# Kernel tuning notes

Measured on AMD Instinct MI355X. Metric: run time of the kernel, lower is better.

The kernel has to match this reference:

```python
import jax, jax.numpy as jnp
import numpy as np

B, T, N, E, H, MAXD = 32, 128, 42, 256, 8, 7
DH = E // H


def _hand_edges():
    left = [(0, 1), (1, 2), (2, 3), (3, 4), (0, 5), (5, 6), (6, 7), (7, 8), (0, 9), (9, 10), (10, 11), (11, 12), (0, 13), (13, 14), (14, 15), (15, 16), (0, 17), (17, 18), (18, 19), (19, 20)]
    right = [(21, 22), (22, 23), (23, 24), (24, 25), (21, 26), (26, 27), (27, 28), (28, 29), (21, 30), (30, 31), (31, 32), (32, 33), (21, 34), (34, 35), (35, 36), (36, 37), (21, 38), (38, 39), (39, 40), (40, 41)]
    tips = [(4, 8), (8, 12), (12, 16), (16, 20), (25, 29), (29, 33), (33, 37), (37, 41)]
    cross = [(0, 21)]
    return left + right + cross + tips


def _graph_constants():
    adj = np.zeros((N, N), dtype=np.float32)
    dist = np.zeros((N, N), dtype=np.float64)
    for a, b in _hand_edges():
        adj[a, b] = 1.0
        adj[b, a] = 1.0
        dist[a, b] = 1.0
        dist[b, a] = 1.0
    # exact replica of the module's single-pass Floyd-Warshall-style loop
    for k in range(N):
        for i in range(N):
            for j in range(N):
                if i != j and dist[i, k] > 0 and dist[k, j] > 0:
                    nd = dist[i, k] + dist[k, j]
                    if dist[i, j] == 0 or nd < dist[i, j]:
                        dist[i, j] = nd
    dist = np.clip(dist, 0, MAXD).astype(np.int32)
    return adj, dist


def setup_inputs() -> dict:
    key = jax.random.key(0)
    ks = jax.random.split(key, 12)
    adj_np, dist_np = _graph_constants()
    s_in = 1.0 / np.sqrt(E)
    return {
        'node_features': jax.random.normal(ks[0], (B, T, N, E), dtype=jnp.float32),
        'adjacency_matrix': jnp.asarray(adj_np),
        'distances': jnp.asarray(dist_np),
        'Wq': jax.random.normal(ks[1], (E, E), dtype=jnp.float32) * s_in,
        'bq': jnp.zeros((E,), dtype=jnp.float32),
        'Wk': jax.random.normal(ks[2], (E, E), dtype=jnp.float32) * s_in,
        'bk': jnp.zeros((E,), dtype=jnp.float32),
        'Wv': jax.random.normal(ks[3], (E, E), dtype=jnp.float32) * s_in,
        'bv': jnp.zeros((E,), dtype=jnp.float32),
        'Wo': jax.random.normal(ks[4], (E, E), dtype=jnp.float32) * s_in,
        'bo': jnp.zeros((E,), dtype=jnp.float32),
        'rel_emb': jax.random.normal(ks[5], (2 * MAXD + 1, H), dtype=jnp.float32) * 0.05,
    }


def reference(node_features, adjacency_matrix, distances, Wq, bq, Wk, bk, Wv, bv, Wo, bo, rel_emb):
    b, t, n, e = node_features.shape
    q = (node_features @ Wq + bq).reshape(b, t, n, H, DH)
    k = (node_features @ Wk + bk).reshape(b, t, n, H, DH)
    v = (node_features @ Wv + bv).reshape(b, t, n, H, DH)
    # scores: [b, t, h, i, j]
    scores = jnp.einsum('btihd,btjhd->bthij', q, k) / jnp.sqrt(jnp.float32(DH))
    # relative position bias: [n, n, h] -> [h, n, n]
    bias = rel_emb[distances]  # (N, N, H)
    scores = scores + jnp.transpose(bias, (2, 0, 1))[None, None]
    mask = (adjacency_matrix > 0).astype(jnp.float32)[None, None, None]
    scores = scores * mask + (1.0 - mask) * (-1e9)
    attn = jax.nn.softmax(scores, axis=-1)
    out = jnp.einsum('bthij,btjhd->btihd', attn, v).reshape(b, t, n, e)
    out = out @ Wo + bo
    return out, attn
```

## Files before the change

### kernel.cpp

```cpp
#include <hip/hip_runtime.h>
#include <stdint.h>


#define TPB 512
constexpr int BT = 4096;
constexpr int N = 42, NP = 48, E = 256, H = 8, DH = 32;
constexpr int NE = N * E;
constexpr int NN = N * N;
constexpr float SCALE = 0.17677669529663687f;

typedef short sh8 __attribute__((ext_vector_type(8)));
typedef float f4 __attribute__((ext_vector_type(4)));

__device__ __forceinline__ float b2f(uint16_t u) {
  union { uint32_t i; float f; } v; v.i = ((uint32_t)u) << 16; return v.f;
}
__device__ __forceinline__ uint16_t f2b(float f) {
  union { float f; uint32_t i; } v; v.f = f;
  const uint32_t x = v.i;
  return (uint16_t)((x + 0x7fffu + ((x >> 16) & 1u)) >> 16);
}

#define SWZ(base, row, cb) \
  ((char*)(base) + ((((row) << 9) + (cb)) ^ (((row) & 7) << 4)))

__global__ __launch_bounds__(256) void wt_kernel(
    const float* __restrict__ Wq, const float* __restrict__ Wk,
    const float* __restrict__ Wv, const float* __restrict__ Wo,
    uint16_t* __restrict__ WT) {
  __shared__ float tl[32][33];
  const int z = blockIdx.z;
  const float* W = (z == 0) ? Wq : (z == 1) ? Wk : (z == 2) ? Wv : Wo;
  uint16_t* dst = WT + z * 65536;
  const int k0 = blockIdx.y * 32, n0 = blockIdx.x * 32;
  const int r = threadIdx.x >> 5, cc = threadIdx.x & 31;
#pragma unroll
  for (int p = 0; p < 4; ++p)
    tl[r + 8 * p][cc] = W[(k0 + r + 8 * p) * E + n0 + cc];
  __syncthreads();
#pragma unroll
  for (int p = 0; p < 4; ++p)
    dst[(n0 + r + 8 * p) * E + k0 + cc] = f2b(tl[cc][r + 8 * p]);
}

__global__ __launch_bounds__(TPB, 4) void gt_kernel(
    const float* __restrict__ X, const float* __restrict__ adj,
    const int* __restrict__ dist,
    const float* __restrict__ bq, const float* __restrict__ bk,
    const float* __restrict__ bv, const float* __restrict__ bo,
    const float* __restrict__ rel, const uint16_t* __restrict__ WT,
    float* __restrict__ out, float* __restrict__ attn) {
  alignas(16) __shared__ char smem[76512];
  uint16_t* const Xb = (uint16_t*)smem;
  uint16_t* const VT = (uint16_t*)smem;
  uint16_t* const Qb = (uint16_t*)(smem + 24576);
  uint16_t* const Kb = (uint16_t*)(smem + 49152);
  uint16_t* const Ps = (uint16_t*)(smem + 24576);
  uint8_t*  const dm8 = (uint8_t*)(smem + 73728);
  float*    const relL = (float*)(smem + 76032);

  const int gid = blockIdx.x;
  const int tid = threadIdx.x;
  const int w = tid >> 6, lane = tid & 63, c = lane & 15, lg = lane >> 4;

  const uint16_t* WTq = WT;
  const uint16_t* WTk = WT + 65536;
  const uint16_t* WTv = WT + 131072;
  const uint16_t* WTo = WT + 196608;

  {
    const float2* Xs = (const float2*)(X + (size_t)gid * NE);
    for (int i = tid; i < NE / 2; i += TPB) {
      const float2 v = Xs[i];
      const int row = i >> 7, cb = (i & 127) << 2;
      const uint32_t pk = (uint32_t)f2b(v.x) | ((uint32_t)f2b(v.y) << 16);
      *(uint32_t*)SWZ(Xb, row, cb) = pk;
    }
    for (int i = tid; i < (NP - N) * 128; i += TPB) {
      const int row = N + (i >> 7), cb = (i & 127) << 2;
      *(uint32_t*)SWZ(Xb, row, cb) = 0u;
    }
    for (int t = tid; t < NP * NP; t += TPB) {
      const int i = t / NP, j = t - i * NP;
      uint8_t v = 0;
      if (i < N && j < N) {
        const float a = adj[i * N + j];
        const int d = dist[i * N + j];
        v = (uint8_t)d | (a > 0.f ? 0x80 : 0);
      }
      dm8[t] = v;
    }
    for (int t = tid; t < 120; t += TPB) relL[t] = rel[t];
  }
  __syncthreads();

  const int nt0 = 2 * w;
  f4 aQ[3][2], aK[3][2], aV[3][2];
#pragma unroll
  for (int mt = 0; mt < 3; ++mt)
#pragma unroll
    for (int nt = 0; nt < 2; ++nt) {
      aQ[mt][nt] = (f4){0.f, 0.f, 0.f, 0.f};
      aK[mt][nt] = (f4){0.f, 0.f, 0.f, 0.f};
      aV[mt][nt] = (f4){0.f, 0.f, 0.f, 0.f};
    }
  for (int kc = 0; kc < E; kc += 32) {
    sh8 xa[3];
#pragma unroll
    for (int mt = 0; mt < 3; ++mt)
      xa[mt] = *(const sh8*)SWZ(Xb, 16 * mt + c, (kc + 8 * lg) * 2);
#pragma unroll
    for (int nt = 0; nt < 2; ++nt) {
      const int n = (nt0 + nt) * 16 + c;
      const int ko = n * E + kc + 8 * lg;
      const sh8 bq8 = *(const sh8*)(WTq + ko);
      const sh8 bk8 = *(const sh8*)(WTk + ko);
      const sh8 bv8 = *(const sh8*)(WTv + ko);
#pragma unroll
      for (int mt = 0; mt < 3; ++mt) {
        aQ[mt][nt] = __builtin_amdgcn_mfma_f32_16x16x32_bf16(xa[mt], bq8, aQ[mt][nt], 0, 0, 0);
        aK[mt][nt] = __builtin_amdgcn_mfma_f32_16x16x32_bf16(xa[mt], bk8, aK[mt][nt], 0, 0, 0);
        aV[mt][nt] = __builtin_amdgcn_mfma_f32_16x16x32_bf16(xa[mt], bv8, aV[mt][nt], 0, 0, 0);
      }
    }
  }
  __syncthreads();

#pragma unroll
  for (int nt = 0; nt < 2; ++nt) {
    const int n = (nt0 + nt) * 16 + c;
    const float bqv = bq[n], bkv = bk[n], bvv = bv[n];
#pragma unroll
    for (int mt = 0; mt < 3; ++mt) {
      uint16_t vr[4];
#pragma unroll
      for (int r = 0; r < 4; ++r) {
        const int i = 16 * mt + 4 * lg + r;
        *(uint16_t*)SWZ(Qb, i, n * 2) = f2b(aQ[mt][nt][r] + bqv);
        *(uint16_t*)SWZ(Kb, i, n * 2) = f2b(aK[mt][nt][r] + bkv);
        vr[r] = f2b(aV[mt][nt][r] + bvv);
      }
      ushort4 vv; vv.x = vr[0]; vv.y = vr[1]; vv.z = vr[2]; vv.w = vr[3];
      *(ushort4*)(VT + n * 48 + 16 * mt + 4 * lg) = vv;
    }
  }
  __syncthreads();

  {
    const int h = w;
    sh8 qa[3], kb8[3];
#pragma unroll
    for (int t = 0; t < 3; ++t) {
      qa[t] = *(const sh8*)SWZ(Qb, 16 * t + c, (h * 32 + 8 * lg) * 2);
      kb8[t] = *(const sh8*)SWZ(Kb, 16 * t + c, (h * 32 + 8 * lg) * 2);
    }
    __syncthreads();

    f4 st[3][3];
#pragma unroll
    for (int mt = 0; mt < 3; ++mt)
#pragma unroll
      for (int nt = 0; nt < 3; ++nt) {
        st[mt][nt] = (f4){0.f, 0.f, 0.f, 0.f};
        st[mt][nt] = __builtin_amdgcn_mfma_f32_16x16x32_bf16(qa[mt], kb8[nt], st[mt][nt], 0, 0, 0);
      }

    uint16_t* Psw = Ps + w * 2688;
#pragma unroll
    for (int mt = 0; mt < 3; ++mt)
#pragma unroll
      for (int r = 0; r < 4; ++r) {
        const int i = 16 * mt + 4 * lg + r;
        float sv[3];
#pragma unroll
        for (int nt = 0; nt < 3; ++nt) {
          const int j = 16 * nt + c;
          const uint8_t dm = dm8[i * NP + j];
          sv[nt] = (dm & 0x80) ? st[mt][nt][r] * SCALE + relL[(dm & 0x7f) * 8 + h]
                               : -1e9f;
        }
        float m = fmaxf(fmaxf(sv[0], sv[1]), sv[2]);
        m = fmaxf(m, __shfl_xor(m, 1));
        m = fmaxf(m, __shfl_xor(m, 2));
        m = fmaxf(m, __shfl_xor(m, 4));
        m = fmaxf(m, __shfl_xor(m, 8));
        float p0 = __expf(sv[0] - m), p1 = __expf(sv[1] - m), p2 = __expf(sv[2] - m);
        float sum = p0 + p1 + p2;
        sum += __shfl_xor(sum, 1);
        sum += __shfl_xor(sum, 2);
        sum += __shfl_xor(sum, 4);
        sum += __shfl_xor(sum, 8);
        const float inv = __builtin_amdgcn_rcpf(sum);
        Psw[i * 56 + 16 * 0 + c] = f2b(p0 * inv);
        Psw[i * 56 + 16 * 1 + c] = f2b(p1 * inv);
        Psw[i * 56 + 16 * 2 + c] = f2b(p2 * inv);
      }

    {
      const size_t abase = ((size_t)gid * H + h) * (size_t)NN;
      for (int p = lane; p < NN; p += 64) {
        const int i = p / N, j = p - i * N;
        attn[abase + p] = b2f(Psw[i * 56 + j]);
      }
    }

    const sh8 z8 = {0, 0, 0, 0, 0, 0, 0, 0};
    sh8 pa0[3], pa1[3], vb0[2], vb1[2];
#pragma unroll
    for (int mt = 0; mt < 3; ++mt) {
      pa0[mt] = *(const sh8*)(Psw + (16 * mt + c) * 56 + 8 * lg);
      pa1[mt] = (lg < 2) ? *(const sh8*)(Psw + (16 * mt + c) * 56 + 32 + 8 * lg) : z8;
    }
#pragma unroll
    for (int nt = 0; nt < 2; ++nt) {
      const int d = h * 32 + 16 * nt + c;
      vb0[nt] = *(const sh8*)(VT + d * 48 + 8 * lg);
      vb1[nt] = (lg < 2) ? *(const sh8*)(VT + d * 48 + 32 + 8 * lg) : z8;
    }
    f4 ov[3][2];
#pragma unroll
    for (int mt = 0; mt < 3; ++mt)
#pragma unroll
      for (int nt = 0; nt < 2; ++nt) {
        ov[mt][nt] = (f4){0.f, 0.f, 0.f, 0.f};
        ov[mt][nt] = __builtin_amdgcn_mfma_f32_16x16x32_bf16(pa0[mt], vb0[nt], ov[mt][nt], 0, 0, 0);
        ov[mt][nt] = __builtin_amdgcn_mfma_f32_16x16x32_bf16(pa1[mt], vb1[nt], ov[mt][nt], 0, 0, 0);
      }
    __syncthreads();
#pragma unroll
    for (int mt = 0; mt < 3; ++mt)
#pragma unroll
      for (int nt = 0; nt < 2; ++nt)
#pragma unroll
        for (int r = 0; r < 4; ++r) {
          const int i = 16 * mt + 4 * lg + r;
          const int dn = h * 32 + 16 * nt + c;
          *(uint16_t*)SWZ(Xb, i, dn * 2) = f2b(ov[mt][nt][r]);
        }
  }
  __syncthreads();

  {
    f4 ao[3][2];
#pragma unroll
    for (int mt = 0; mt < 3; ++mt)
#pragma unroll
      for (int nt = 0; nt < 2; ++nt) ao[mt][nt] = (f4){0.f, 0.f, 0.f, 0.f};
    for (int kc = 0; kc < E; kc += 32) {
      sh8 xa[3];
#pragma unroll
      for (int mt = 0; mt < 3; ++mt)
        xa[mt] = *(const sh8*)SWZ(Xb, 16 * mt + c, (kc + 8 * lg) * 2);
#pragma unroll
      for (int nt = 0; nt < 2; ++nt) {
        const int n = (nt0 + nt) * 16 + c;
        const sh8 b8 = *(const sh8*)(WTo + n * E + kc + 8 * lg);
#pragma unroll
        for (int mt = 0; mt < 3; ++mt)
          ao[mt][nt] = __builtin_amdgcn_mfma_f32_16x16x32_bf16(xa[mt], b8, ao[mt][nt], 0, 0, 0);
      }
    }
#pragma unroll
    for (int nt = 0; nt < 2; ++nt) {
      const int n = (nt0 + nt) * 16 + c;
      const float bov = bo[n];
#pragma unroll
      for (int mt = 0; mt < 3; ++mt)
#pragma unroll
        for (int r = 0; r < 4; ++r) {
          const int i = 16 * mt + 4 * lg + r;
          if (i < N) out[(size_t)gid * NE + i * E + n] = ao[mt][nt][r] + bov;
        }
    }
  }
}

extern "C" void kernel_launch(void* const* d_in, const int* in_sizes, int n_in,
                              void* d_out, int out_size, void* d_ws, size_t ws_size,
                              hipStream_t stream) {
  const float* X    = (const float*)d_in[0];
  const float* adj  = (const float*)d_in[1];
  const int*   dist = (const int*)d_in[2];
  const float* Wq   = (const float*)d_in[3];
  const float* bq   = (const float*)d_in[4];
  const float* Wk   = (const float*)d_in[5];
  const float* bk   = (const float*)d_in[6];
  const float* Wv   = (const float*)d_in[7];
  const float* bv   = (const float*)d_in[8];
  const float* Wo   = (const float*)d_in[9];
  const float* bo   = (const float*)d_in[10];
  const float* rel  = (const float*)d_in[11];
  float* out  = (float*)d_out;
  float* attn = out + (size_t)BT * NE;
  uint16_t* WT = (uint16_t*)d_ws;

  wt_kernel<<<dim3(8, 8, 4), dim3(256), 0, stream>>>(Wq, Wk, Wv, Wo, WT);
  gt_kernel<<<dim3(BT), dim3(TPB), 0, stream>>>(
      X, adj, dist, bq, bk, bv, bo, rel, WT, out, attn);
}
```

Baseline: 439.6 us.

## Split QKV projection into sequential passes with per-wave Q/K transpose scratch

The fused QKV projection that held three accumulator sets is replaced by three sequential GEMM passes. Each Q and K result is transposed through a small per-wave LDS scratch straight into MFMA fragments, which removes the shared Q/K buffers and one block barrier and cuts LDS use. The score MFMA is transposed (K times Q) so each lane holds a whole row slice and softmax needs only two cross-lane shuffles. Bf16 conversion now uses the hardware v_cvt_pk_bf16_f32 instruction, and X is loaded as float4. The attn store is moved after the PV MFMAs, and it still reads Psw with the old 56-element row stride, which matches the new 112-byte row pitch.

Result: slower. 535.7 us (+21.9%).

```diff
diff --git a/kernel.cpp b/kernel.cpp
--- a/kernel.cpp
+++ b/kernel.cpp
@@ -4,7 +4,7 @@
 
 #define TPB 512
 constexpr int BT = 4096;
-constexpr int N = 42, NP = 48, E = 256, H = 8, DH = 32;
+constexpr int N = 42, NP = 48, E = 256, H = 8;
 constexpr int NE = N * E;
 constexpr int NN = N * N;
 constexpr float SCALE = 0.17677669529663687f;
@@ -12,13 +12,14 @@
 typedef short sh8 __attribute__((ext_vector_type(8)));
 typedef float f4 __attribute__((ext_vector_type(4)));
 
+__device__ __forceinline__ uint32_t cvtpk(float lo, float hi) {
+  uint32_t d;
+  asm("v_cvt_pk_bf16_f32 %0, %1, %2" : "=v"(d) : "v"(lo), "v"(hi));
+  return d;
+}
+__device__ __forceinline__ uint16_t f2b1(float f) { return (uint16_t)cvtpk(f, f); }
 __device__ __forceinline__ float b2f(uint16_t u) {
   union { uint32_t i; float f; } v; v.i = ((uint32_t)u) << 16; return v.f;
-}
-__device__ __forceinline__ uint16_t f2b(float f) {
-  union { float f; uint32_t i; } v; v.f = f;
-  const uint32_t x = v.i;
-  return (uint16_t)((x + 0x7fffu + ((x >> 16) & 1u)) >> 16);
 }
 
 #define SWZ(base, row, cb) \
@@ -40,7 +41,45 @@
   __syncthreads();
 #pragma unroll
   for (int p = 0; p < 4; ++p)
-    dst[(n0 + r + 8 * p) * E + k0 + cc] = f2b(tl[cc][r + 8 * p]);
+    dst[(n0 + r + 8 * p) * E + k0 + cc] = f2b1(tl[cc][r + 8 * p]);
+}
+
+__device__ __forceinline__ void gemm_pass(const uint16_t* __restrict__ Wt,
+                                          const char* Xb, int c, int lg, int nt0,
+                                          f4 acc[3][2]) {
+#pragma unroll
+  for (int mt = 0; mt < 3; ++mt)
+#pragma unroll
+    for (int nt = 0; nt < 2; ++nt) acc[mt][nt] = (f4){0.f, 0.f, 0.f, 0.f};
+  for (int kc = 0; kc < E; kc += 32) {
+    sh8 xa[3];
+#pragma unroll
+    for (int mt = 0; mt < 3; ++mt)
+      xa[mt] = *(const sh8*)SWZ(Xb, 16 * mt + c, (kc + 8 * lg) * 2);
+#pragma unroll
+    for (int nt = 0; nt < 2; ++nt) {
+      const sh8 b8 = *(const sh8*)(Wt + ((nt0 + nt) * 16 + c) * E + kc + 8 * lg);
+#pragma unroll
+      for (int mt = 0; mt < 3; ++mt)
+        acc[mt][nt] = __builtin_amdgcn_mfma_f32_16x16x32_bf16(xa[mt], b8, acc[mt][nt], 0, 0, 0);
+    }
+  }
+}
+
+__device__ __forceinline__ void tr_qk(const f4 acc[3][2], const float* __restrict__ bias,
+                                      int n0, int c, int lg, uint16_t* scr, sh8 fr[3]) {
+#pragma unroll
+  for (int nt = 0; nt < 2; ++nt) {
+    const float bv = bias[n0 + 16 * nt + c];
+#pragma unroll
+    for (int mt = 0; mt < 3; ++mt)
+#pragma unroll
+      for (int r = 0; r < 4; ++r)
+        scr[(16 * mt + 4 * lg + r) * 40 + 16 * nt + c] = f2b1(acc[mt][nt][r] + bv);
+  }
+#pragma unroll
+  for (int mt = 0; mt < 3; ++mt)
+    fr[mt] = *(const sh8*)(scr + (16 * mt + c) * 40 + 8 * lg);
 }
 
 __global__ __launch_bounds__(TPB, 4) void gt_kernel(
@@ -50,43 +89,35 @@
     const float* __restrict__ bv, const float* __restrict__ bo,
     const float* __restrict__ rel, const uint16_t* __restrict__ WT,
     float* __restrict__ out, float* __restrict__ attn) {
-  alignas(16) __shared__ char smem[76512];
-  uint16_t* const Xb = (uint16_t*)smem;
+  alignas(16) __shared__ char smem[70368];
+  char* const Xb = smem;
   uint16_t* const VT = (uint16_t*)smem;
-  uint16_t* const Qb = (uint16_t*)(smem + 24576);
-  uint16_t* const Kb = (uint16_t*)(smem + 49152);
-  uint16_t* const Ps = (uint16_t*)(smem + 24576);
-  uint8_t*  const dm8 = (uint8_t*)(smem + 73728);
-  float*    const relL = (float*)(smem + 76032);
+  uint8_t*  const dm8 = (uint8_t*)(smem + 67584);
+  float*    const relL = (float*)(smem + 69888);
 
   const int gid = blockIdx.x;
   const int tid = threadIdx.x;
   const int w = tid >> 6, lane = tid & 63, c = lane & 15, lg = lane >> 4;
-
-  const uint16_t* WTq = WT;
-  const uint16_t* WTk = WT + 65536;
-  const uint16_t* WTv = WT + 131072;
-  const uint16_t* WTo = WT + 196608;
-
-  {
-    const float2* Xs = (const float2*)(X + (size_t)gid * NE);
-    for (int i = tid; i < NE / 2; i += TPB) {
-      const float2 v = Xs[i];
-      const int row = i >> 7, cb = (i & 127) << 2;
-      const uint32_t pk = (uint32_t)f2b(v.x) | ((uint32_t)f2b(v.y) << 16);
-      *(uint32_t*)SWZ(Xb, row, cb) = pk;
-    }
-    for (int i = tid; i < (NP - N) * 128; i += TPB) {
-      const int row = N + (i >> 7), cb = (i & 127) << 2;
-      *(uint32_t*)SWZ(Xb, row, cb) = 0u;
+  const int nt0 = 2 * w, n0 = 32 * w;
+  uint16_t* const scr = (uint16_t*)(smem + 24576 + w * 5376);
+
+  {
+    const float4* Xs = (const float4*)(X + (size_t)gid * NE);
+    for (int i = tid; i < NE / 4; i += TPB) {
+      const float4 v = Xs[i];
+      uint2 pk; pk.x = cvtpk(v.x, v.y); pk.y = cvtpk(v.z, v.w);
+      *(uint2*)SWZ(Xb, i >> 6, (i & 63) << 3) = pk;
+    }
+    for (int i = tid; i < (NP - N) * 32; i += TPB) {
+      uint2 z; z.x = 0u; z.y = 0u;
+      *(uint2*)SWZ(Xb, N + (i >> 5), (i & 31) << 3) = z;
     }
     for (int t = tid; t < NP * NP; t += TPB) {
       const int i = t / NP, j = t - i * NP;
       uint8_t v = 0;
       if (i < N && j < N) {
         const float a = adj[i * N + j];
-        const int d = dist[i * N + j];
-        v = (uint8_t)d | (a > 0.f ? 0x80 : 0);
+        v = (uint8_t)dist[i * N + j] | (a > 0.f ? 0x80 : 0);
       }
       dm8[t] = v;
     }
@@ -94,113 +125,74 @@
   }
   __syncthreads();
 
-  const int nt0 = 2 * w;
-  f4 aQ[3][2], aK[3][2], aV[3][2];
-#pragma unroll
-  for (int mt = 0; mt < 3; ++mt)
-#pragma unroll
-    for (int nt = 0; nt < 2; ++nt) {
-      aQ[mt][nt] = (f4){0.f, 0.f, 0.f, 0.f};
-      aK[mt][nt] = (f4){0.f, 0.f, 0.f, 0.f};
-      aV[mt][nt] = (f4){0.f, 0.f, 0.f, 0.f};
-    }
-  for (int kc = 0; kc < E; kc += 32) {
-    sh8 xa[3];
-#pragma unroll
-    for (int mt = 0; mt < 3; ++mt)
-      xa[mt] = *(const sh8*)SWZ(Xb, 16 * mt + c, (kc + 8 * lg) * 2);
-#pragma unroll
-    for (int nt = 0; nt < 2; ++nt) {
-      const int n = (nt0 + nt) * 16 + c;
-      const int ko = n * E + kc + 8 * lg;
-      const sh8 bq8 = *(const sh8*)(WTq + ko);
-      const sh8 bk8 = *(const sh8*)(WTk + ko);
-      const sh8 bv8 = *(const sh8*)(WTv + ko);
-#pragma unroll
-      for (int mt = 0; mt < 3; ++mt) {
-        aQ[mt][nt] = __builtin_amdgcn_mfma_f32_16x16x32_bf16(xa[mt], bq8, aQ[mt][nt], 0, 0, 0);
-        aK[mt][nt] = __builtin_amdgcn_mfma_f32_16x16x32_bf16(xa[mt], bk8, aK[mt][nt], 0, 0, 0);
-        aV[mt][nt] = __builtin_amdgcn_mfma_f32_16x16x32_bf16(xa[mt], bv8, aV[mt][nt], 0, 0, 0);
-      }
-    }
-  }
+  sh8 qa[3], kb[3];
+  {
+    f4 acc[3][2];
+    gemm_pass(WT, Xb, c, lg, nt0, acc);
+    tr_qk(acc, bq, n0, c, lg, scr, qa);
+    gemm_pass(WT + 65536, Xb, c, lg, nt0, acc);
+    tr_qk(acc, bk, n0, c, lg, scr, kb);
+  }
+  f4 av[3][2];
+  gemm_pass(WT + 131072, Xb, c, lg, nt0, av);
   __syncthreads();
 
 #pragma unroll
   for (int nt = 0; nt < 2; ++nt) {
-    const int n = (nt0 + nt) * 16 + c;
-    const float bqv = bq[n], bkv = bk[n], bvv = bv[n];
+    const int n = n0 + 16 * nt + c;
+    const float bvv = bv[n];
 #pragma unroll
     for (int mt = 0; mt < 3; ++mt) {
-      uint16_t vr[4];
-#pragma unroll
-      for (int r = 0; r < 4; ++r) {
-        const int i = 16 * mt + 4 * lg + r;
-        *(uint16_t*)SWZ(Qb, i, n * 2) = f2b(aQ[mt][nt][r] + bqv);
-        *(uint16_t*)SWZ(Kb, i, n * 2) = f2b(aK[mt][nt][r] + bkv);
-        vr[r] = f2b(aV[mt][nt][r] + bvv);
-      }
-      ushort4 vv; vv.x = vr[0]; vv.y = vr[1]; vv.z = vr[2]; vv.w = vr[3];
-      *(ushort4*)(VT + n * 48 + 16 * mt + 4 * lg) = vv;
-    }
-  }
-  __syncthreads();
+      uint2 pk;
+      pk.x = cvtpk(av[mt][nt][0] + bvv, av[mt][nt][1] + bvv);
+      pk.y = cvtpk(av[mt][nt][2] + bvv, av[mt][nt][3] + bvv);
+      *(uint2*)((char*)VT + n * 96 + 32 * mt + 8 * lg) = pk;
+    }
+  }
 
   {
     const int h = w;
-    sh8 qa[3], kb8[3];
-#pragma unroll
-    for (int t = 0; t < 3; ++t) {
-      qa[t] = *(const sh8*)SWZ(Qb, 16 * t + c, (h * 32 + 8 * lg) * 2);
-      kb8[t] = *(const sh8*)SWZ(Kb, 16 * t + c, (h * 32 + 8 * lg) * 2);
-    }
-    __syncthreads();
-
     f4 st[3][3];
 #pragma unroll
     for (int mt = 0; mt < 3; ++mt)
 #pragma unroll
       for (int nt = 0; nt < 3; ++nt) {
         st[mt][nt] = (f4){0.f, 0.f, 0.f, 0.f};
-        st[mt][nt] = __builtin_amdgcn_mfma_f32_16x16x32_bf16(qa[mt], kb8[nt], st[mt][nt], 0, 0, 0);
-      }
-
-    uint16_t* Psw = Ps + w * 2688;
-#pragma unroll
-    for (int mt = 0; mt < 3; ++mt)
-#pragma unroll
-      for (int r = 0; r < 4; ++r) {
-        const int i = 16 * mt + 4 * lg + r;
-        float sv[3];
-#pragma unroll
-        for (int nt = 0; nt < 3; ++nt) {
-          const int j = 16 * nt + c;
+        st[mt][nt] = __builtin_amdgcn_mfma_f32_16x16x32_bf16(kb[mt], qa[nt], st[mt][nt], 0, 0, 0);
+      }
+
+    uint16_t* const Psw = scr;
+#pragma unroll
+    for (int nt = 0; nt < 3; ++nt) {
+      const int i = 16 * nt + c;
+      float sv[12];
+#pragma unroll
+      for (int mt = 0; mt < 3; ++mt)
+#pragma unroll
+        for (int r = 0; r < 4; ++r) {
+          const int j = 16 * mt + 4 * lg + r;
           const uint8_t dm = dm8[i * NP + j];
-          sv[nt] = (dm & 0x80) ? st[mt][nt][r] * SCALE + relL[(dm & 0x7f) * 8 + h]
-                               : -1e9f;
+          const float s = st[mt][nt][r] * SCALE + relL[(dm & 0x7f) * 8 + h];
+          sv[mt * 4 + r] = (dm & 0x80) ? s : -1e9f;
         }
-        float m = fmaxf(fmaxf(sv[0], sv[1]), sv[2]);
-        m = fmaxf(m, __shfl_xor(m, 1));
-        m = fmaxf(m, __shfl_xor(m, 2));
-        m = fmaxf(m, __shfl_xor(m, 4));
-        m = fmaxf(m, __shfl_xor(m, 8));
-        float p0 = __expf(sv[0] - m), p1 = __expf(sv[1] - m), p2 = __expf(sv[2] - m);
-        float sum = p0 + p1 + p2;
-        sum += __shfl_xor(sum, 1);
-        sum += __shfl_xor(sum, 2);
-        sum += __shfl_xor(sum, 4);
-        sum += __shfl_xor(sum, 8);
-        const float inv = __builtin_amdgcn_rcpf(sum);
-        Psw[i * 56 + 16 * 0 + c] = f2b(p0 * inv);
-        Psw[i * 56 + 16 * 1 + c] = f2b(p1 * inv);
-        Psw[i * 56 + 16 * 2 + c] = f2b(p2 * inv);
-      }
-
-    {
-      const size_t abase = ((size_t)gid * H + h) * (size_t)NN;
-      for (int p = lane; p < NN; p += 64) {
-        const int i = p / N, j = p - i * N;
-        attn[abase + p] = b2f(Psw[i * 56 + j]);
+      float m = sv[0];
+#pragma unroll
+      for (int k = 1; k < 12; ++k) m = fmaxf(m, sv[k]);
+      m = fmaxf(m, __shfl_xor(m, 16));
+      m = fmaxf(m, __shfl_xor(m, 32));
+      float p[12], sum = 0.f;
+#pragma unroll
+      for (int k = 0; k < 12; ++k) { p[k] = __expf(sv[k] - m); sum += p[k]; }
+      sum += __shfl_xor(sum, 16);
+      sum += __shfl_xor(sum, 32);
+      const float inv = __builtin_amdgcn_rcpf(sum);
+#pragma unroll
+      for (int mt = 0; mt < 3; ++mt) {
+        const uint32_t d0 = cvtpk(p[mt * 4 + 0] * inv, p[mt * 4 + 1] * inv);
+        const uint32_t d1 = cvtpk(p[mt * 4 + 2] * inv, p[mt * 4 + 3] * inv);
+        char* base = (char*)Psw + i * 112 + 32 * mt + 8 * lg;
+        *(uint32_t*)base = d0;
+        *(uint32_t*)(base + 4) = d1;
       }
     }
 
@@ -208,14 +200,15 @@
     sh8 pa0[3], pa1[3], vb0[2], vb1[2];
 #pragma unroll
     for (int mt = 0; mt < 3; ++mt) {
-      pa0[mt] = *(const sh8*)(Psw + (16 * mt + c) * 56 + 8 * lg);
-      pa1[mt] = (lg < 2) ? *(const sh8*)(Psw + (16 * mt + c) * 56 + 32 + 8 * lg) : z8;
+      char* base = (char*)Psw + (16 * mt + c) * 112;
+      pa0[mt] = *(const sh8*)(base + 16 * lg);
+      pa1[mt] = (lg < 2) ? *(const sh8*)(base + 64 + 16 * lg) : z8;
     }
 #pragma unroll
     for (int nt = 0; nt < 2; ++nt) {
-      const int d = h * 32 + 16 * nt + c;
-      vb0[nt] = *(const sh8*)(VT + d * 48 + 8 * lg);
-      vb1[nt] = (lg < 2) ? *(const sh8*)(VT + d * 48 + 32 + 8 * lg) : z8;
+      char* base = (char*)VT + (n0 + 16 * nt + c) * 96;
+      vb0[nt] = *(const sh8*)(base + 16 * lg);
+      vb1[nt] = (lg < 2) ? *(const sh8*)(base + 64 + 16 * lg) : z8;
     }
     f4 ov[3][2];
 #pragma unroll
@@ -226,43 +219,31 @@
         ov[mt][nt] = __builtin_amdgcn_mfma_f32_16x16x32_bf16(pa0[mt], vb0[nt], ov[mt][nt], 0, 0, 0);
         ov[mt][nt] = __builtin_amdgcn_mfma_f32_16x16x32_bf16(pa1[mt], vb1[nt], ov[mt][nt], 0, 0, 0);
       }
+
+    const size_t abase = ((size_t)gid * H + h) * (size_t)NN;
+    for (int p = lane; p < NN; p += 64) {
+      const int i = p / N, j = p - i * N;
+      attn[abase + p] = b2f(Psw[i * 56 + j]);
+    }
     __syncthreads();
+
 #pragma unroll
     for (int mt = 0; mt < 3; ++mt)
 #pragma unroll
       for (int nt = 0; nt < 2; ++nt)
 #pragma unroll
-        for (int r = 0; r < 4; ++r) {
-          const int i = 16 * mt + 4 * lg + r;
-          const int dn = h * 32 + 16 * nt + c;
-          *(uint16_t*)SWZ(Xb, i, dn * 2) = f2b(ov[mt][nt][r]);
-        }
+        for (int r = 0; r < 4; ++r)
+          *(uint16_t*)SWZ(Xb, 16 * mt + 4 * lg + r, (n0 + 16 * nt + c) * 2) =
+              f2b1(ov[mt][nt][r]);
   }
   __syncthreads();
 
   {
     f4 ao[3][2];
-#pragma unroll
-    for (int mt = 0; mt < 3; ++mt)
-#pragma unroll
-      for (int nt = 0; nt < 2; ++nt) ao[mt][nt] = (f4){0.f, 0.f, 0.f, 0.f};
-    for (int kc = 0; kc < E; kc += 32) {
-      sh8 xa[3];
-#pragma unroll
-      for (int mt = 0; mt < 3; ++mt)
-        xa[mt] = *(const sh8*)SWZ(Xb, 16 * mt + c, (kc + 8 * lg) * 2);
-#pragma unroll
-      for (int nt = 0; nt < 2; ++nt) {
-        const int n = (nt0 + nt) * 16 + c;
-        const sh8 b8 = *(const sh8*)(WTo + n * E + kc + 8 * lg);
-#pragma unroll
-        for (int mt = 0; mt < 3; ++mt)
-          ao[mt][nt] = __builtin_amdgcn_mfma_f32_16x16x32_bf16(xa[mt], b8, ao[mt][nt], 0, 0, 0);
-      }
-    }
+    gemm_pass(WT + 196608, Xb, c, lg, nt0, ao);
 #pragma unroll
     for (int nt = 0; nt < 2; ++nt) {
-      const int n = (nt0 + nt) * 16 + c;
+      const int n = n0 + 16 * nt + c;
       const float bov = bo[n];
 #pragma unroll
       for (int mt = 0; mt < 3; ++mt)
```
